# Optimization experiments

Measured on AMD Instinct MI355X. Metric: run time of the kernel, lower is better.

Reference implementation:

```python
import jax, jax.numpy as jnp
import numpy as np

P_X, P_H, P_L, P_VT, P_ET, B = 512, 1024, 4, 512, 256, 512
IN_DIM = P_X + 2 * P_H  # concat([x, prev_time_h, prev_layer_h])


def setup_inputs() -> dict:
    key = jax.random.key(0)
    ks = jax.random.split(key, 10)
    sc_in = 1.0 / np.sqrt(IN_DIM)
    sc_lh = 1.0 / np.sqrt(P_L * P_H)
    return {
        "input_x": jax.random.normal(ks[0], (B, P_X), jnp.float32),
        "h_prev": jax.random.normal(ks[1], (P_L, B, P_H), jnp.float32),
        "c_prev": jax.random.normal(ks[2], (P_L, B, P_H), jnp.float32),
        # stacked gate weights: [L, 4 gates (i,f,o,s), h, in_dim]
        "Wg": jax.random.uniform(ks[3], (P_L, 4, P_H, IN_DIM), jnp.float32, -sc_in, sc_in),
        "bg": jax.random.uniform(ks[4], (P_L, 4, P_H), jnp.float32, -sc_in, sc_in),
        "W_y": jax.random.uniform(ks[5], (P_VT, P_L * P_H), jnp.float32, -sc_lh, sc_lh),
        "b_y": jax.random.uniform(ks[6], (P_VT,), jnp.float32, -sc_lh, sc_lh),
        "W_E": jax.random.uniform(ks[7], (P_ET, P_L * P_H), jnp.float32, -sc_lh, sc_lh),
        "b_E": jax.random.uniform(ks[8], (P_ET,), jnp.float32, -sc_lh, sc_lh),
    }


def _controller(input_x, h_prev, c_prev, Wg, bg):
    prev_layer = jnp.zeros((input_x.shape[0], P_H), input_x.dtype)
    hiddens = []
    for i in range(P_L):  # loop over small fixed layer count
        z = jnp.concatenate([input_x, h_prev[i], prev_layer], axis=-1)  # [B, IN_DIM]
        g = jnp.einsum("bd,ghd->bgh", z, Wg[i]) + bg[i]  # [B, 4, H], one fused GEMM
        i_g = jax.nn.sigmoid(g[:, 0])
        f_g = jax.nn.sigmoid(g[:, 1])
        o_g = jax.nn.sigmoid(g[:, 2])
        s_g = jnp.tanh(g[:, 3])
        c_new = f_g * c_prev[i] + i_g * s_g
        h_new = o_g * jnp.tanh(c_new)
        hiddens.append(h_new)
        prev_layer = h_new
    return jnp.concatenate(hiddens, axis=-1)  # [B, L*H]


def reference(input_x, h_prev, c_prev, Wg, bg, W_y, b_y, W_E, b_E):
    hidden = _controller(input_x, h_prev, c_prev, Wg, bg)
    output = hidden @ W_y.T + b_y      # [B, v_t]
    interface = hidden @ W_E.T + b_E   # [B, E_t]
    return (output, interface)
```

## Files before the change

### kernel.cpp

```cpp
#include <hip/hip_runtime.h>


typedef short    shortx8  __attribute__((ext_vector_type(8)));
typedef float    floatx16 __attribute__((ext_vector_type(16)));

__device__ __forceinline__ unsigned int f2bf1(float x) {
  unsigned int u = __float_as_uint(x);
  return (u + 0x7fffu + ((u >> 16) & 1u)) >> 16;
}
__device__ __forceinline__ unsigned int f2bf2(float lo, float hi) {
  return f2bf1(lo) | (f2bf1(hi) << 16);
}
__device__ __forceinline__ float sigm(float x) { return 1.f / (1.f + __expf(-x)); }
__device__ __forceinline__ float tanh_(float x) { return 1.f - 2.f / (__expf(2.f * x) + 1.f); }

__global__ __launch_bounds__(256) void prep_a0(const float* __restrict__ x,
                                               const float* __restrict__ hp,
                                               unsigned short* __restrict__ A0) {
  const int l   = blockIdx.y;
  const int idx = blockIdx.x * 256 + threadIdx.x;
  const int b   = idx / 192;
  const int kk  = (idx - b * 192) * 8;
  float v[8];
  if (kk < 512) {
    const float* s = x + (size_t)b * 512 + kk;
#pragma unroll
    for (int i = 0; i < 8; ++i) v[i] = s[i];
  } else {
    const float* s = hp + ((size_t)l * 512 + b) * 1024 + (kk - 512);
#pragma unroll
    for (int i = 0; i < 8; ++i) v[i] = s[i];
  }
  uint4 o;
  o.x = f2bf2(v[0], v[1]); o.y = f2bf2(v[2], v[3]);
  o.z = f2bf2(v[4], v[5]); o.w = f2bf2(v[6], v[7]);
  *(uint4*)(A0 + ((size_t)l * 512 + b) * 1536 + kk) = o;
}

__global__ __launch_bounds__(256, 2) void gemm_gates(
    const unsigned short* __restrict__ A0, const float* __restrict__ Wg,
    const float* __restrict__ bg, float* __restrict__ G) {
  __shared__ __align__(16) unsigned short As[2][128 * 64];
  __shared__ __align__(16) unsigned short Bs[2][128 * 64];
  const int tid = threadIdx.x, lane = tid & 63, wave = tid >> 6;
  const int raw   = blockIdx.x + 4 * (blockIdx.y + 32 * blockIdx.z);
  const int xcd   = raw & 7, slot = raw >> 3;
  const int nl    = (slot >> 2) * 8 + xcd;
  const int mbase = (slot & 3) * 128;
  const int nbase = (nl & 31) * 128;
  const int l     = nl >> 5;
  const unsigned short* Ab = A0 + ((size_t)l * 512 + mbase) * 1536;
  const float*          Bb = Wg + (size_t)l * 4096 * 2560 + (size_t)nbase * 2560;
  const int arow = wave * 8 + (lane >> 3);
  const int akg  = lane & 7;

  uint4  apf[4];
  float4 bpf[8];
  auto loadT = [&](int kt) {
    const int kg = kt * 64;
#pragma unroll
    for (int r = 0; r < 4; ++r)
      apf[r] = *(const uint4*)(Ab + (size_t)(arow + r * 32) * 1536 + kg + akg * 8);
#pragma unroll
    for (int j = 0; j < 8; ++j) {
      const int idx = j * 256 + tid;
      bpf[j] = *(const float4*)(Bb + (size_t)(idx >> 4) * 2560 + kg + (idx & 15) * 4);
    }
  };
  auto storeT = [&](int buf) {
#pragma unroll
    for (int r = 0; r < 4; ++r) {
      const int row = arow + r * 32;
      *(uint4*)(&As[buf][row * 64 + ((akg ^ (row & 7)) * 8)]) = apf[r];
    }
#pragma unroll
    for (int j = 0; j < 8; ++j) {
      const int idx = j * 256 + tid;
      const int n = idx >> 4, kc = (idx & 15) * 4;
      uint2 pk;
      pk.x = f2bf2(bpf[j].x, bpf[j].y);
      pk.y = f2bf2(bpf[j].z, bpf[j].w);
      *(uint2*)(&Bs[buf][n * 64 + (((kc >> 3) ^ (n & 7)) * 8) + (kc & 4)]) = pk;
    }
  };

  floatx16 acc[2][2];
#pragma unroll
  for (int a = 0; a < 2; ++a)
#pragma unroll
    for (int b2 = 0; b2 < 2; ++b2)
#pragma unroll
      for (int r = 0; r < 16; ++r) acc[a][b2][r] = 0.f;

  const int wm = (wave >> 1) * 64, wn = (wave & 1) * 64;
  loadT(0);
  storeT(0);
  __syncthreads();
  for (int kt = 0; kt < 24; ++kt) {
    if (kt + 1 < 24) loadT(kt + 1);
    const int cb = kt & 1;
#pragma unroll
    for (int ks = 0; ks < 4; ++ks) {
      const int gb = ks * 2 + (lane >> 5);
      shortx8 af[2], bfv[2];
#pragma unroll
      for (int sm = 0; sm < 2; ++sm) {
        const int row = wm + sm * 32 + (lane & 31);
        af[sm] = *(const shortx8*)(&As[cb][row * 64 + ((gb ^ (row & 7)) * 8)]);
      }
#pragma unroll
      for (int sn = 0; sn < 2; ++sn) {
        const int row = wn + sn * 32 + (lane & 31);
        bfv[sn] = *(const shortx8*)(&Bs[cb][row * 64 + ((gb ^ (row & 7)) * 8)]);
      }
#pragma unroll
      for (int sm = 0; sm < 2; ++sm)
#pragma unroll
        for (int sn = 0; sn < 2; ++sn)
          acc[sm][sn] = __builtin_amdgcn_mfma_f32_32x32x16_bf16(
              af[sm], bfv[sn], acc[sm][sn], 0, 0, 0);
    }
    if (kt + 1 < 24) storeT((kt + 1) & 1);
    __syncthreads();
  }

  const float* bgl = bg + (size_t)l * 4096;
  float* Gl = G + ((size_t)l * 512 + mbase) * 4096;
#pragma unroll
  for (int sm = 0; sm < 2; ++sm)
#pragma unroll
    for (int sn = 0; sn < 2; ++sn) {
      const int col = nbase + wn + sn * 32 + (lane & 31);
      const float bias = bgl[col];
#pragma unroll
      for (int r = 0; r < 16; ++r) {
        const int row = wm + sm * 32 + ((r & 3) + 8 * (r >> 2) + 4 * (lane >> 5));
        Gl[(size_t)row * 4096 + col] = acc[sm][sn][r] + bias;
      }
    }
}

__global__ __launch_bounds__(256) void cell0(const float* __restrict__ G,
                                             const float* __restrict__ cp_l,
                                             unsigned short* __restrict__ hidden) {
  const int idx = (blockIdx.x * 256 + threadIdx.x) * 4;
  const int b = idx >> 10, h = idx & 1023;
  const float* g0 = G + (size_t)b * 4096;
  const float4 vi = *(const float4*)(g0 + h);
  const float4 vf = *(const float4*)(g0 + 1024 + h);
  const float4 vo = *(const float4*)(g0 + 2048 + h);
  const float4 vs = *(const float4*)(g0 + 3072 + h);
  const float4 cp = *(const float4*)(cp_l + (size_t)b * 1024 + h);
  const float gi[4] = {vi.x, vi.y, vi.z, vi.w};
  const float gf[4] = {vf.x, vf.y, vf.z, vf.w};
  const float go[4] = {vo.x, vo.y, vo.z, vo.w};
  const float gs[4] = {vs.x, vs.y, vs.z, vs.w};
  const float cc[4] = {cp.x, cp.y, cp.z, cp.w};
  float hn[4];
#pragma unroll
  for (int j = 0; j < 4; ++j) {
    const float c = sigm(gf[j]) * cc[j] + sigm(gi[j]) * tanh_(gs[j]);
    hn[j] = sigm(go[j]) * tanh_(c);
  }
  uint2 o;
  o.x = f2bf2(hn[0], hn[1]);
  o.y = f2bf2(hn[2], hn[3]);
  *(uint2*)(hidden + (size_t)b * 4096 + h) = o;
}

__global__ __launch_bounds__(512, 2) void gemm_seq_cell(
    const unsigned short* __restrict__ hidden_ro, const float* __restrict__ Wg,
    const float* __restrict__ G, const float* __restrict__ c_prev,
    unsigned short* __restrict__ hidden_w, int l) {
  __shared__ __align__(16) unsigned char raw_lds[49152];
  unsigned short* As = (unsigned short*)raw_lds;
  unsigned short* Bs = (unsigned short*)(raw_lds + 32768);
  float*          Gex = (float*)raw_lds;
  const int tid = threadIdx.x, lane = tid & 63, wave = tid >> 6;
  const int rawb  = blockIdx.x + 4 * blockIdx.y;
  const int xcd   = rawb & 7, slot = rawb >> 3;
  const int mbase = (slot & 3) * 128;
  const int h0    = ((slot >> 2) * 8 + xcd) * 16;
  const unsigned short* Ab = hidden_ro + (size_t)(l - 1) * 1024;
  const float*          Bl = Wg + (size_t)l * 4096 * 2560 + 1536;

  uint4  apf[2];
  float4 bpf[2];
  auto loadT = [&](int kt) {
    const int kg = kt * 64;
#pragma unroll
    for (int r = 0; r < 2; ++r) {
      const int row = (tid >> 3) + r * 64;
      apf[r] = *(const uint4*)(Ab + (size_t)(mbase + row) * 4096 + kg + (tid & 7) * 8);
    }
#pragma unroll
    for (int j = 0; j < 2; ++j) {
      const int idx = j * 512 + tid;
      const int nl = idx >> 4, kc = (idx & 15) * 4;
      const int grow = (nl >> 4) * 1024 + h0 + (nl & 15);
      bpf[j] = *(const float4*)(Bl + (size_t)grow * 2560 + kg + kc);
    }
  };
  auto storeT = [&](int buf) {
#pragma unroll
    for (int r = 0; r < 2; ++r) {
      const int row = (tid >> 3) + r * 64;
      *(uint4*)(&As[buf * 8192 + row * 64 + (((tid & 7) ^ (row & 7)) * 8)]) = apf[r];
    }
#pragma unroll
    for (int j = 0; j < 2; ++j) {
      const int idx = j * 512 + tid;
      const int nl = idx >> 4, kc = (idx & 15) * 4;
      uint2 pk;
      pk.x = f2bf2(bpf[j].x, bpf[j].y);
      pk.y = f2bf2(bpf[j].z, bpf[j].w);
      *(uint2*)(&Bs[buf * 4096 + nl * 64 + (((kc >> 3) ^ (nl & 7)) * 8) + (kc & 4)]) = pk;
    }
  };

  floatx16 acc;
#pragma unroll
  for (int r = 0; r < 16; ++r) acc[r] = 0.f;
  const int wm = (wave & 3) * 32, wn = (wave >> 2) * 32;

  loadT(0);
  storeT(0);
  __syncthreads();
  for (int kt = 0; kt < 16; ++kt) {
    if (kt + 1 < 16) loadT(kt + 1);
    const int cb = kt & 1;
    const int rowa = wm + (lane & 31);
    const int rowb = wn + (lane & 31);
#pragma unroll
    for (int ks = 0; ks < 4; ++ks) {
      const int gb = ks * 2 + (lane >> 5);
      const shortx8 af = *(const shortx8*)(&As[cb * 8192 + rowa * 64 + ((gb ^ (rowa & 7)) * 8)]);
      const shortx8 bfv = *(const shortx8*)(&Bs[cb * 4096 + rowb * 64 + ((gb ^ (rowb & 7)) * 8)]);
      acc = __builtin_amdgcn_mfma_f32_32x32x16_bf16(af, bfv, acc, 0, 0, 0);
    }
    if (kt + 1 < 16) storeT((kt + 1) & 1);
    __syncthreads();
  }

  {
    const int col = wn + (lane & 31);
#pragma unroll
    for (int r = 0; r < 16; ++r) {
      const int row = wm + ((r & 3) + 8 * (r >> 2) + 4 * (lane >> 5));
      Gex[row * 65 + col] = acc[r];
    }
  }
  __syncthreads();

  const int hh = tid & 15, q = tid >> 4;
#pragma unroll
  for (int bi = 0; bi < 4; ++bi) {
    const int bl = bi * 32 + q;
    const int b  = mbase + bl;
    const int hg = h0 + hh;
    const float* Gb = G + ((size_t)l * 512 + b) * 4096;
    float gv[4];
#pragma unroll
    for (int g = 0; g < 4; ++g)
      gv[g] = Gex[bl * 65 + g * 16 + hh] + Gb[g * 1024 + hg];
    const float c_old = c_prev[((size_t)l * 512 + b) * 1024 + hg];
    const float c  = sigm(gv[1]) * c_old + sigm(gv[0]) * tanh_(gv[3]);
    const float hn = sigm(gv[2]) * tanh_(c);
    hidden_w[(size_t)b * 4096 + l * 1024 + hg] = (unsigned short)f2bf1(hn);
  }
}

__global__ __launch_bounds__(256) void gemm_heads(
    const unsigned short* __restrict__ A, const float* __restrict__ Wy,
    const float* __restrict__ WE, float* __restrict__ Cp) {
  __shared__ __align__(16) unsigned short As[2][128 * 64];
  __shared__ __align__(16) unsigned short Bs[2][128 * 64];
  const int tid = threadIdx.x, lane = tid & 63, wave = tid >> 6;
  const int rawb = blockIdx.x + 8 * (blockIdx.y + 6 * blockIdx.z);
  const int xcd  = rawb & 7, slot = rawb >> 3;
  const int pair = (slot >> 2) * 8 + xcd;
  const int mbase  = (slot & 3) * 128;
  const int ksplit = pair & 7;
  const int nt     = pair >> 3;
  const int nbase  = nt * 128;
  const float* Bb = (nt < 4) ? (Wy + (size_t)nbase * 4096)
                             : (WE + (size_t)(nbase - 512) * 4096);
  const int k0 = ksplit * 512;
  const unsigned short* Ab = A + (size_t)mbase * 4096;
  const int arow = wave * 8 + (lane >> 3);
  const int akg  = lane & 7;

  uint4  apf[4];
  float4 bpf[8];
  auto loadT = [&](int kt) {
    const int kg = k0 + kt * 64;
#pragma unroll
    for (int r = 0; r < 4; ++r)
      apf[r] = *(const uint4*)(Ab + (size_t)(arow + r * 32) * 4096 + kg + akg * 8);
#pragma unroll
    for (int j = 0; j < 8; ++j) {
      const int idx = j * 256 + tid;
      bpf[j] = *(const float4*)(Bb + (size_t)(idx >> 4) * 4096 + kg + (idx & 15) * 4);
    }
  };
  auto storeT = [&](int buf) {
#pragma unroll
    for (int r = 0; r < 4; ++r) {
      const int row = arow + r * 32;
      *(uint4*)(&As[buf][row * 64 + ((akg ^ (row & 7)) * 8)]) = apf[r];
    }
#pragma unroll
    for (int j = 0; j < 8; ++j) {
      const int idx = j * 256 + tid;
      const int n = idx >> 4, kc = (idx & 15) * 4;
      uint2 pk;
      pk.x = f2bf2(bpf[j].x, bpf[j].y);
      pk.y = f2bf2(bpf[j].z, bpf[j].w);
      *(uint2*)(&Bs[buf][n * 64 + (((kc >> 3) ^ (n & 7)) * 8) + (kc & 4)]) = pk;
    }
  };

  floatx16 acc[2][2];
#pragma unroll
  for (int a = 0; a < 2; ++a)
#pragma unroll
    for (int b2 = 0; b2 < 2; ++b2)
#pragma unroll
      for (int r = 0; r < 16; ++r) acc[a][b2][r] = 0.f;
  const int wm = (wave >> 1) * 64, wn = (wave & 1) * 64;

  loadT(0);
  storeT(0);
  __syncthreads();
  for (int kt = 0; kt < 8; ++kt) {
    if (kt + 1 < 8) loadT(kt + 1);
    const int cb = kt & 1;
#pragma unroll
    for (int ks = 0; ks < 4; ++ks) {
      const int gb = ks * 2 + (lane >> 5);
      shortx8 af[2], bfv[2];
#pragma unroll
      for (int sm = 0; sm < 2; ++sm) {
        const int row = wm + sm * 32 + (lane & 31);
        af[sm] = *(const shortx8*)(&As[cb][row * 64 + ((gb ^ (row & 7)) * 8)]);
      }
#pragma unroll
      for (int sn = 0; sn < 2; ++sn) {
        const int row = wn + sn * 32 + (lane & 31);
        bfv[sn] = *(const shortx8*)(&Bs[cb][row * 64 + ((gb ^ (row & 7)) * 8)]);
      }
#pragma unroll
      for (int sm = 0; sm < 2; ++sm)
#pragma unroll
        for (int sn = 0; sn < 2; ++sn)
          acc[sm][sn] = __builtin_amdgcn_mfma_f32_32x32x16_bf16(
              af[sm], bfv[sn], acc[sm][sn], 0, 0, 0);
    }
    if (kt + 1 < 8) storeT((kt + 1) & 1);
    __syncthreads();
  }

  float* Co = Cp + (size_t)ksplit * 512 * 768;
#pragma unroll
  for (int sm = 0; sm < 2; ++sm)
#pragma unroll
    for (int sn = 0; sn < 2; ++sn) {
      const int col = nbase + wn + sn * 32 + (lane & 31);
#pragma unroll
      for (int r = 0; r < 16; ++r) {
        const int row = mbase + wm + sm * 32 +
                        ((r & 3) + 8 * (r >> 2) + 4 * (lane >> 5));
        Co[(size_t)row * 768 + col] = acc[sm][sn][r];
      }
    }
}

__global__ __launch_bounds__(256) void head_reduce(
    const float* __restrict__ hp, const float* __restrict__ b_y,
    const float* __restrict__ b_E, float* __restrict__ out) {
  const int n = blockIdx.x * 256 + threadIdx.x;
  const int b = blockIdx.y;
  float s = 0.f;
#pragma unroll
  for (int ks = 0; ks < 8; ++ks)
    s += hp[(size_t)ks * 512 * 768 + (size_t)b * 768 + n];
  if (n < 512)
    out[(size_t)b * 512 + n] = s + b_y[n];
  else
    out[(size_t)512 * 512 + (size_t)b * 256 + (n - 512)] = s + b_E[n - 512];
}

extern "C" void kernel_launch(void* const* d_in, const int* in_sizes, int n_in,
                              void* d_out, int out_size, void* d_ws, size_t ws_size,
                              hipStream_t stream) {
  const float* x      = (const float*)d_in[0];
  const float* h_prev = (const float*)d_in[1];
  const float* c_prev = (const float*)d_in[2];
  const float* Wg     = (const float*)d_in[3];
  const float* bg     = (const float*)d_in[4];
  const float* W_y    = (const float*)d_in[5];
  const float* b_y    = (const float*)d_in[6];
  const float* W_E    = (const float*)d_in[7];
  const float* b_E    = (const float*)d_in[8];

  char* ws = (char*)d_ws;
  unsigned short* A0     = (unsigned short*)(ws + 0);
  float*          G      = (float*)(ws + 6291456);
  unsigned short* hidden = (unsigned short*)(ws + 39845888);
  float*          hpart  = (float*)(ws + 44040192);

  prep_a0<<<dim3(384, 4), 256, 0, stream>>>(x, h_prev, A0);
  gemm_gates<<<dim3(4, 32, 4), 256, 0, stream>>>(A0, Wg, bg, G);
  cell0<<<512, 256, 0, stream>>>(G, c_prev, hidden);
  for (int l = 1; l < 4; ++l)
    gemm_seq_cell<<<dim3(4, 64), 512, 0, stream>>>(hidden, Wg, G, c_prev,
                                                   hidden, l);
  gemm_heads<<<dim3(8, 6, 4), 256, 0, stream>>>(hidden, W_y, W_E, hpart);
  head_reduce<<<dim3(3, 512), 256, 0, stream>>>(hpart, b_y, b_E, (float*)d_out);
}
```

Before: 420.4 us.

## Prefetch two K-tiles ahead in GEMMs and enlarge gate GEMM tile to 256x128

All three GEMM kernels now keep two register prefetch sets and load tiles two steps ahead, with a manually double-unrolled main loop, to hide more global-load latency behind the MFMA work. The gate GEMM is also restructured to 512 threads with a 256x128 output tile and a 1-D grid of 256 blocks. The grid maps one layer and M half to each XCD so each XCD reuses the same A rows. This costs more registers and LDS per block, which may lower occupancy, and the gate grid shrinks from 512 to 256 blocks.

```diff
diff --git a/kernel.cpp b/kernel.cpp
--- a/kernel.cpp
+++ b/kernel.cpp
@@ -37,50 +37,50 @@
   *(uint4*)(A0 + ((size_t)l * 512 + b) * 1536 + kk) = o;
 }
 
-__global__ __launch_bounds__(256, 2) void gemm_gates(
+__global__ __launch_bounds__(512, 2) void gemm_gates(
     const unsigned short* __restrict__ A0, const float* __restrict__ Wg,
     const float* __restrict__ bg, float* __restrict__ G) {
-  __shared__ __align__(16) unsigned short As[2][128 * 64];
+  __shared__ __align__(16) unsigned short As[2][256 * 64];
   __shared__ __align__(16) unsigned short Bs[2][128 * 64];
   const int tid = threadIdx.x, lane = tid & 63, wave = tid >> 6;
-  const int raw   = blockIdx.x + 4 * (blockIdx.y + 32 * blockIdx.z);
-  const int xcd   = raw & 7, slot = raw >> 3;
-  const int nl    = (slot >> 2) * 8 + xcd;
-  const int mbase = (slot & 3) * 128;
-  const int nbase = (nl & 31) * 128;
-  const int l     = nl >> 5;
+  const int bid   = blockIdx.x;
+  const int xcd   = bid & 7;
+  const int n     = bid >> 3;
+  const int l     = xcd >> 1;
+  const int mbase = (xcd & 1) * 256;
+  const int nbase = n * 128;
   const unsigned short* Ab = A0 + ((size_t)l * 512 + mbase) * 1536;
   const float*          Bb = Wg + (size_t)l * 4096 * 2560 + (size_t)nbase * 2560;
-  const int arow = wave * 8 + (lane >> 3);
-  const int akg  = lane & 7;
-
-  uint4  apf[4];
-  float4 bpf[8];
-  auto loadT = [&](int kt) {
+  const int arow = tid >> 3;
+  const int akg  = tid & 7;
+
+  uint4  apfA[4], apfB[4];
+  float4 bpfA[4], bpfB[4];
+  auto loadT = [&](uint4 (&ap)[4], float4 (&bp)[4], int kt) {
     const int kg = kt * 64;
 #pragma unroll
     for (int r = 0; r < 4; ++r)
-      apf[r] = *(const uint4*)(Ab + (size_t)(arow + r * 32) * 1536 + kg + akg * 8);
-#pragma unroll
-    for (int j = 0; j < 8; ++j) {
-      const int idx = j * 256 + tid;
-      bpf[j] = *(const float4*)(Bb + (size_t)(idx >> 4) * 2560 + kg + (idx & 15) * 4);
-    }
-  };
-  auto storeT = [&](int buf) {
+      ap[r] = *(const uint4*)(Ab + (size_t)(arow + r * 64) * 1536 + kg + akg * 8);
+#pragma unroll
+    for (int j = 0; j < 4; ++j) {
+      const int idx = j * 512 + tid;
+      bp[j] = *(const float4*)(Bb + (size_t)(idx >> 4) * 2560 + kg + (idx & 15) * 4);
+    }
+  };
+  auto storeT = [&](uint4 (&ap)[4], float4 (&bp)[4], int buf) {
 #pragma unroll
     for (int r = 0; r < 4; ++r) {
-      const int row = arow + r * 32;
-      *(uint4*)(&As[buf][row * 64 + ((akg ^ (row & 7)) * 8)]) = apf[r];
-    }
-#pragma unroll
-    for (int j = 0; j < 8; ++j) {
-      const int idx = j * 256 + tid;
-      const int n = idx >> 4, kc = (idx & 15) * 4;
+      const int row = arow + r * 64;
+      *(uint4*)(&As[buf][row * 64 + ((akg ^ (row & 7)) * 8)]) = ap[r];
+    }
+#pragma unroll
+    for (int j = 0; j < 4; ++j) {
+      const int idx = j * 512 + tid;
+      const int nr = idx >> 4, kc = (idx & 15) * 4;
       uint2 pk;
-      pk.x = f2bf2(bpf[j].x, bpf[j].y);
-      pk.y = f2bf2(bpf[j].z, bpf[j].w);
-      *(uint2*)(&Bs[buf][n * 64 + (((kc >> 3) ^ (n & 7)) * 8) + (kc & 4)]) = pk;
+      pk.x = f2bf2(bp[j].x, bp[j].y);
+      pk.y = f2bf2(bp[j].z, bp[j].w);
+      *(uint2*)(&Bs[buf][nr * 64 + (((kc >> 3) ^ (nr & 7)) * 8) + (kc & 4)]) = pk;
     }
   };
 
@@ -92,13 +92,8 @@
 #pragma unroll
       for (int r = 0; r < 16; ++r) acc[a][b2][r] = 0.f;
 
-  const int wm = (wave >> 1) * 64, wn = (wave & 1) * 64;
-  loadT(0);
-  storeT(0);
-  __syncthreads();
-  for (int kt = 0; kt < 24; ++kt) {
-    if (kt + 1 < 24) loadT(kt + 1);
-    const int cb = kt & 1;
+  const int wm = (wave & 3) * 64, wn = (wave >> 2) * 64;
+  auto compute = [&](int cb) {
 #pragma unroll
     for (int ks = 0; ks < 4; ++ks) {
       const int gb = ks * 2 + (lane >> 5);
@@ -120,7 +115,22 @@
           acc[sm][sn] = __builtin_amdgcn_mfma_f32_32x32x16_bf16(
               af[sm], bfv[sn], acc[sm][sn], 0, 0, 0);
     }
-    if (kt + 1 < 24) storeT((kt + 1) & 1);
+  };
+
+  loadT(apfA, bpfA, 0);
+  loadT(apfB, bpfB, 1);
+  storeT(apfA, bpfA, 0);
+  __syncthreads();
+#pragma unroll 1
+  for (int kt2 = 0; kt2 < 12; ++kt2) {
+    const int kt = kt2 * 2;
+    if (kt + 2 < 24) loadT(apfA, bpfA, kt + 2);
+    compute(0);
+    storeT(apfB, bpfB, 1);
+    __syncthreads();
+    if (kt + 3 < 24) loadT(apfB, bpfB, kt + 3);
+    compute(1);
+    if (kt + 2 < 24) storeT(apfA, bpfA, 0);
     __syncthreads();
   }
 
@@ -184,36 +194,36 @@
   const unsigned short* Ab = hidden_ro + (size_t)(l - 1) * 1024;
   const float*          Bl = Wg + (size_t)l * 4096 * 2560 + 1536;
 
-  uint4  apf[2];
-  float4 bpf[2];
-  auto loadT = [&](int kt) {
+  uint4  apfA[2], apfB[2];
+  float4 bpfA[2], bpfB[2];
+  auto loadT = [&](uint4 (&ap)[2], float4 (&bp)[2], int kt) {
     const int kg = kt * 64;
 #pragma unroll
     for (int r = 0; r < 2; ++r) {
       const int row = (tid >> 3) + r * 64;
-      apf[r] = *(const uint4*)(Ab + (size_t)(mbase + row) * 4096 + kg + (tid & 7) * 8);
+      ap[r] = *(const uint4*)(Ab + (size_t)(mbase + row) * 4096 + kg + (tid & 7) * 8);
     }
 #pragma unroll
     for (int j = 0; j < 2; ++j) {
       const int idx = j * 512 + tid;
       const int nl = idx >> 4, kc = (idx & 15) * 4;
       const int grow = (nl >> 4) * 1024 + h0 + (nl & 15);
-      bpf[j] = *(const float4*)(Bl + (size_t)grow * 2560 + kg + kc);
-    }
-  };
-  auto storeT = [&](int buf) {
+      bp[j] = *(const float4*)(Bl + (size_t)grow * 2560 + kg + kc);
+    }
+  };
+  auto storeT = [&](uint4 (&ap)[2], float4 (&bp)[2], int buf) {
 #pragma unroll
     for (int r = 0; r < 2; ++r) {
       const int row = (tid >> 3) + r * 64;
-      *(uint4*)(&As[buf * 8192 + row * 64 + (((tid & 7) ^ (row & 7)) * 8)]) = apf[r];
+      *(uint4*)(&As[buf * 8192 + row * 64 + (((tid & 7) ^ (row & 7)) * 8)]) = ap[r];
     }
 #pragma unroll
     for (int j = 0; j < 2; ++j) {
       const int idx = j * 512 + tid;
       const int nl = idx >> 4, kc = (idx & 15) * 4;
       uint2 pk;
-      pk.x = f2bf2(bpf[j].x, bpf[j].y);
-      pk.y = f2bf2(bpf[j].z, bpf[j].w);
+      pk.x = f2bf2(bp[j].x, bp[j].y);
+      pk.y = f2bf2(bp[j].z, bp[j].w);
       *(uint2*)(&Bs[buf * 4096 + nl * 64 + (((kc >> 3) ^ (nl & 7)) * 8) + (kc & 4)]) = pk;
     }
   };
@@ -222,15 +232,10 @@
 #pragma unroll
   for (int r = 0; r < 16; ++r) acc[r] = 0.f;
   const int wm = (wave & 3) * 32, wn = (wave >> 2) * 32;
-
-  loadT(0);
-  storeT(0);
-  __syncthreads();
-  for (int kt = 0; kt < 16; ++kt) {
-    if (kt + 1 < 16) loadT(kt + 1);
-    const int cb = kt & 1;
-    const int rowa = wm + (lane & 31);
-    const int rowb = wn + (lane & 31);
+  const int rowa = wm + (lane & 31);
+  const int rowb = wn + (lane & 31);
+
+  auto compute = [&](int cb) {
 #pragma unroll
     for (int ks = 0; ks < 4; ++ks) {
       const int gb = ks * 2 + (lane >> 5);
@@ -238,7 +243,22 @@
       const shortx8 bfv = *(const shortx8*)(&Bs[cb * 4096 + rowb * 64 + ((gb ^ (rowb & 7)) * 8)]);
       acc = __builtin_amdgcn_mfma_f32_32x32x16_bf16(af, bfv, acc, 0, 0, 0);
     }
-    if (kt + 1 < 16) storeT((kt + 1) & 1);
+  };
+
+  loadT(apfA, bpfA, 0);
+  loadT(apfB, bpfB, 1);
+  storeT(apfA, bpfA, 0);
+  __syncthreads();
+#pragma unroll 1
+  for (int kt2 = 0; kt2 < 8; ++kt2) {
+    const int kt = kt2 * 2;
+    if (kt + 2 < 16) loadT(apfA, bpfA, kt + 2);
+    compute(0);
+    storeT(apfB, bpfB, 1);
+    __syncthreads();
+    if (kt + 3 < 16) loadT(apfB, bpfB, kt + 3);
+    compute(1);
+    if (kt + 2 < 16) storeT(apfA, bpfA, 0);
     __syncthreads();
   }
 
@@ -270,7 +290,7 @@
   }
 }
 
-__global__ __launch_bounds__(256) void gemm_heads(
+__global__ __launch_bounds__(256, 2) void gemm_heads(
     const unsigned short* __restrict__ A, const float* __restrict__ Wy,
     const float* __restrict__ WE, float* __restrict__ Cp) {
   __shared__ __align__(16) unsigned short As[2][128 * 64];
@@ -290,32 +310,32 @@
   const int arow = wave * 8 + (lane >> 3);
   const int akg  = lane & 7;
 
-  uint4  apf[4];
-  float4 bpf[8];
-  auto loadT = [&](int kt) {
+  uint4  apfA[4], apfB[4];
+  float4 bpfA[8], bpfB[8];
+  auto loadT = [&](uint4 (&ap)[4], float4 (&bp)[8], int kt) {
     const int kg = k0 + kt * 64;
 #pragma unroll
     for (int r = 0; r < 4; ++r)
-      apf[r] = *(const uint4*)(Ab + (size_t)(arow + r * 32) * 4096 + kg + akg * 8);
+      ap[r] = *(const uint4*)(Ab + (size_t)(arow + r * 32) * 4096 + kg + akg * 8);
 #pragma unroll
     for (int j = 0; j < 8; ++j) {
       const int idx = j * 256 + tid;
-      bpf[j] = *(const float4*)(Bb + (size_t)(idx >> 4) * 4096 + kg + (idx & 15) * 4);
-    }
-  };
-  auto storeT = [&](int buf) {
+      bp[j] = *(const float4*)(Bb + (size_t)(idx >> 4) * 4096 + kg + (idx & 15) * 4);
+    }
+  };
+  auto storeT = [&](uint4 (&ap)[4], float4 (&bp)[8], int buf) {
 #pragma unroll
     for (int r = 0; r < 4; ++r) {
       const int row = arow + r * 32;
-      *(uint4*)(&As[buf][row * 64 + ((akg ^ (row & 7)) * 8)]) = apf[r];
+      *(uint4*)(&As[buf][row * 64 + ((akg ^ (row & 7)) * 8)]) = ap[r];
     }
 #pragma unroll
     for (int j = 0; j < 8; ++j) {
       const int idx = j * 256 + tid;
       const int n = idx >> 4, kc = (idx & 15) * 4;
       uint2 pk;
-      pk.x = f2bf2(bpf[j].x, bpf[j].y);
-      pk.y = f2bf2(bpf[j].z, bpf[j].w);
+      pk.x = f2bf2(bp[j].x, bp[j].y);
+      pk.y = f2bf2(bp[j].z, bp[j].w);
       *(uint2*)(&Bs[buf][n * 64 + (((kc >> 3) ^ (n & 7)) * 8) + (kc & 4)]) = pk;
     }
   };
@@ -329,12 +349,7 @@
       for (int r = 0; r < 16; ++r) acc[a][b2][r] = 0.f;
   const int wm = (wave >> 1) * 64, wn = (wave & 1) * 64;
 
-  loadT(0);
-  storeT(0);
-  __syncthreads();
-  for (int kt = 0; kt < 8; ++kt) {
-    if (kt + 1 < 8) loadT(kt + 1);
-    const int cb = kt & 1;
+  auto compute = [&](int cb) {
 #pragma unroll
     for (int ks = 0; ks < 4; ++ks) {
       const int gb = ks * 2 + (lane >> 5);
@@ -356,7 +371,22 @@
           acc[sm][sn] = __builtin_amdgcn_mfma_f32_32x32x16_bf16(
               af[sm], bfv[sn], acc[sm][sn], 0, 0, 0);
     }
-    if (kt + 1 < 8) storeT((kt + 1) & 1);
+  };
+
+  loadT(apfA, bpfA, 0);
+  loadT(apfB, bpfB, 1);
+  storeT(apfA, bpfA, 0);
+  __syncthreads();
+#pragma unroll 1
+  for (int kt2 = 0; kt2 < 4; ++kt2) {
+    const int kt = kt2 * 2;
+    if (kt + 2 < 8) loadT(apfA, bpfA, kt + 2);
+    compute(0);
+    storeT(apfB, bpfB, 1);
+    __syncthreads();
+    if (kt + 3 < 8) loadT(apfB, bpfB, kt + 3);
+    compute(1);
+    if (kt + 2 < 8) storeT(apfA, bpfA, 0);
     __syncthreads();
   }
 
@@ -410,7 +440,7 @@
   float*          hpart  = (float*)(ws + 44040192);
 
   prep_a0<<<dim3(384, 4), 256, 0, stream>>>(x, h_prev, A0);
-  gemm_gates<<<dim3(4, 32, 4), 256, 0, stream>>>(A0, Wg, bg, G);
+  gemm_gates<<<dim3(256), 512, 0, stream>>>(A0, Wg, bg, G);
   cell0<<<512, 256, 0, stream>>>(G, c_prev, hidden);
   for (int l = 1; l < 4; ++l)
     gemm_seq_cell<<<dim3(4, 64), 512, 0, stream>>>(hidden, Wg, G, c_prev,
```

After: 444.9 us. +5.8%, slower.

## Pre-convert sequential-layer weights to bf16 and stream them in LDS-free kernel

Applied to the files above, without the earlier changes.

Adds a kernel that converts the previous-layer slice of the gate weights for layers 1-3 into a compact bf16 buffer each call. The per-layer sequential GEMM+cell kernel is replaced by an LDS-free version: each wave computes a 16x16 tile per gate with 16x16x32 bf16 MFMA, prefetching operands from global memory into registers four k-steps ahead. This removes the fp32 weight loads with in-loop conversion, the LDS staging and the block barriers, and uses more blocks. In exchange it adds an extra conversion pass over the weights and puts the bf16 buffer in the same workspace region as hpart, which is safe only because the head GEMM runs after it on the same stream.

```diff
diff --git a/kernel.cpp b/kernel.cpp
--- a/kernel.cpp
+++ b/kernel.cpp
@@ -2,6 +2,7 @@
 
 
 typedef short    shortx8  __attribute__((ext_vector_type(8)));
+typedef float    floatx4  __attribute__((ext_vector_type(4)));
 typedef float    floatx16 __attribute__((ext_vector_type(16)));
 
 __device__ __forceinline__ unsigned int f2bf1(float x) {
@@ -35,6 +36,22 @@
   o.x = f2bf2(v[0], v[1]); o.y = f2bf2(v[2], v[3]);
   o.z = f2bf2(v[4], v[5]); o.w = f2bf2(v[6], v[7]);
   *(uint4*)(A0 + ((size_t)l * 512 + b) * 1536 + kk) = o;
+}
+
+__global__ __launch_bounds__(256) void conv_wseq(const float* __restrict__ Wg,
+                                                 unsigned short* __restrict__ Wseq) {
+  const int idx = blockIdx.x * 256 + threadIdx.x;
+  const int row = idx >> 7;
+  const int k0  = (idx & 127) * 8;
+  const int l   = (row >> 12) + 1;
+  const int n   = row & 4095;
+  const float* s = Wg + (size_t)l * 4096 * 2560 + (size_t)n * 2560 + 1536 + k0;
+  const float4 v0 = *(const float4*)(s);
+  const float4 v1 = *(const float4*)(s + 4);
+  uint4 o;
+  o.x = f2bf2(v0.x, v0.y); o.y = f2bf2(v0.z, v0.w);
+  o.z = f2bf2(v1.x, v1.y); o.w = f2bf2(v1.z, v1.w);
+  *(uint4*)(Wseq + (size_t)row * 1024 + k0) = o;
 }
 
 __global__ __launch_bounds__(256, 2) void gemm_gates(
@@ -168,105 +185,93 @@
   *(uint2*)(hidden + (size_t)b * 4096 + h) = o;
 }
 
-__global__ __launch_bounds__(512, 2) void gemm_seq_cell(
-    const unsigned short* __restrict__ hidden_ro, const float* __restrict__ Wg,
+__global__ __launch_bounds__(256) void seq_stream(
+    const unsigned short* __restrict__ hidden_ro,
+    const unsigned short* __restrict__ Wseq,
     const float* __restrict__ G, const float* __restrict__ c_prev,
     unsigned short* __restrict__ hidden_w, int l) {
-  __shared__ __align__(16) unsigned char raw_lds[49152];
-  unsigned short* As = (unsigned short*)raw_lds;
-  unsigned short* Bs = (unsigned short*)(raw_lds + 32768);
-  float*          Gex = (float*)raw_lds;
-  const int tid = threadIdx.x, lane = tid & 63, wave = tid >> 6;
-  const int rawb  = blockIdx.x + 4 * blockIdx.y;
-  const int xcd   = rawb & 7, slot = rawb >> 3;
-  const int mbase = (slot & 3) * 128;
-  const int h0    = ((slot >> 2) * 8 + xcd) * 16;
-  const unsigned short* Ab = hidden_ro + (size_t)(l - 1) * 1024;
-  const float*          Bl = Wg + (size_t)l * 4096 * 2560 + 1536;
-
-  uint4  apf[2];
-  float4 bpf[2];
-  auto loadT = [&](int kt) {
-    const int kg = kt * 64;
-#pragma unroll
-    for (int r = 0; r < 2; ++r) {
-      const int row = (tid >> 3) + r * 64;
-      apf[r] = *(const uint4*)(Ab + (size_t)(mbase + row) * 4096 + kg + (tid & 7) * 8);
-    }
-#pragma unroll
-    for (int j = 0; j < 2; ++j) {
-      const int idx = j * 512 + tid;
-      const int nl = idx >> 4, kc = (idx & 15) * 4;
-      const int grow = (nl >> 4) * 1024 + h0 + (nl & 15);
-      bpf[j] = *(const float4*)(Bl + (size_t)grow * 2560 + kg + kc);
-    }
-  };
-  auto storeT = [&](int buf) {
-#pragma unroll
-    for (int r = 0; r < 2; ++r) {
-      const int row = (tid >> 3) + r * 64;
-      *(uint4*)(&As[buf * 8192 + row * 64 + (((tid & 7) ^ (row & 7)) * 8)]) = apf[r];
-    }
-#pragma unroll
-    for (int j = 0; j < 2; ++j) {
-      const int idx = j * 512 + tid;
-      const int nl = idx >> 4, kc = (idx & 15) * 4;
-      uint2 pk;
-      pk.x = f2bf2(bpf[j].x, bpf[j].y);
-      pk.y = f2bf2(bpf[j].z, bpf[j].w);
-      *(uint2*)(&Bs[buf * 4096 + nl * 64 + (((kc >> 3) ^ (nl & 7)) * 8) + (kc & 4)]) = pk;
-    }
-  };
-
-  floatx16 acc;
-#pragma unroll
-  for (int r = 0; r < 16; ++r) acc[r] = 0.f;
-  const int wm = (wave & 3) * 32, wn = (wave >> 2) * 32;
-
-  loadT(0);
-  storeT(0);
-  __syncthreads();
-  for (int kt = 0; kt < 16; ++kt) {
-    if (kt + 1 < 16) loadT(kt + 1);
-    const int cb = kt & 1;
-    const int rowa = wm + (lane & 31);
-    const int rowb = wn + (lane & 31);
-#pragma unroll
-    for (int ks = 0; ks < 4; ++ks) {
-      const int gb = ks * 2 + (lane >> 5);
-      const shortx8 af = *(const shortx8*)(&As[cb * 8192 + rowa * 64 + ((gb ^ (rowa & 7)) * 8)]);
-      const shortx8 bfv = *(const shortx8*)(&Bs[cb * 4096 + rowb * 64 + ((gb ^ (rowb & 7)) * 8)]);
-      acc = __builtin_amdgcn_mfma_f32_32x32x16_bf16(af, bfv, acc, 0, 0, 0);
-    }
-    if (kt + 1 < 16) storeT((kt + 1) & 1);
-    __syncthreads();
-  }
-
-  {
-    const int col = wn + (lane & 31);
-#pragma unroll
-    for (int r = 0; r < 16; ++r) {
-      const int row = wm + ((r & 3) + 8 * (r >> 2) + 4 * (lane >> 5));
-      Gex[row * 65 + col] = acc[r];
-    }
-  }
-  __syncthreads();
-
-  const int hh = tid & 15, q = tid >> 4;
-#pragma unroll
-  for (int bi = 0; bi < 4; ++bi) {
-    const int bl = bi * 32 + q;
-    const int b  = mbase + bl;
-    const int hg = h0 + hh;
-    const float* Gb = G + ((size_t)l * 512 + b) * 4096;
-    float gv[4];
-#pragma unroll
-    for (int g = 0; g < 4; ++g)
-      gv[g] = Gex[bl * 65 + g * 16 + hh] + Gb[g * 1024 + hg];
-    const float c_old = c_prev[((size_t)l * 512 + b) * 1024 + hg];
-    const float c  = sigm(gv[1]) * c_old + sigm(gv[0]) * tanh_(gv[3]);
-    const float hn = sigm(gv[2]) * tanh_(c);
-    hidden_w[(size_t)b * 4096 + l * 1024 + hg] = (unsigned short)f2bf1(hn);
+  const int tid = threadIdx.x, lane = tid & 63, wv = tid >> 6;
+  const int bid = blockIdx.x;
+  const int x   = bid & 7;
+  const int mg  = (bid >> 3) & 7;
+  const int t   = bid >> 6;
+  const int ht  = x * 8 + t;
+  const int mt  = mg * 4 + wv;
+  const int mb  = mt * 16, h0 = ht * 16;
+  const int lrow = lane & 15, lg = lane >> 4;
+
+  const unsigned short* Ab = hidden_ro + (size_t)(mb + lrow) * 4096
+                             + (size_t)(l - 1) * 1024 + lg * 8;
+  const unsigned short* Bb = Wseq + (size_t)(l - 1) * 4194304
+                             + (size_t)(h0 + lrow) * 1024 + lg * 8;
+
+  const int brow = mb + lg * 4;
+  const int hg   = h0 + lrow;
+  float gvv[4][4];
+  float cold[4];
+#pragma unroll
+  for (int r = 0; r < 4; ++r) {
+    const float* Gb = G + ((size_t)l * 512 + brow + r) * 4096 + hg;
+#pragma unroll
+    for (int g = 0; g < 4; ++g) gvv[g][r] = Gb[g * 1024];
+    cold[r] = c_prev[((size_t)l * 512 + brow + r) * 1024 + hg];
+  }
+
+  floatx4 acc0, acc1, acc2, acc3;
+#pragma unroll
+  for (int r = 0; r < 4; ++r) { acc0[r] = 0.f; acc1[r] = 0.f; acc2[r] = 0.f; acc3[r] = 0.f; }
+
+  shortx8 a0, a1, a2, a3;
+  shortx8 b00, b01, b02, b03;
+  shortx8 b10, b11, b12, b13;
+  shortx8 b20, b21, b22, b23;
+  shortx8 b30, b31, b32, b33;
+
+#define LD_SET(ai, b0_, b1_, b2_, b3_, kt)                                   \
+  {                                                                          \
+    const int ko = (kt) * 32;                                                \
+    ai  = *(const shortx8*)(Ab + ko);                                        \
+    b0_ = *(const shortx8*)(Bb + ko);                                        \
+    b1_ = *(const shortx8*)(Bb + 1048576 + ko);                              \
+    b2_ = *(const shortx8*)(Bb + 2097152 + ko);                              \
+    b3_ = *(const shortx8*)(Bb + 3145728 + ko);                              \
+  }
+#define C_SET(ai, b0_, b1_, b2_, b3_)                                        \
+  {                                                                          \
+    acc0 = __builtin_amdgcn_mfma_f32_16x16x32_bf16(ai, b0_, acc0, 0, 0, 0);  \
+    acc1 = __builtin_amdgcn_mfma_f32_16x16x32_bf16(ai, b1_, acc1, 0, 0, 0);  \
+    acc2 = __builtin_amdgcn_mfma_f32_16x16x32_bf16(ai, b2_, acc2, 0, 0, 0);  \
+    acc3 = __builtin_amdgcn_mfma_f32_16x16x32_bf16(ai, b3_, acc3, 0, 0, 0);  \
+  }
+
+  LD_SET(a0, b00, b01, b02, b03, 0)
+  LD_SET(a1, b10, b11, b12, b13, 1)
+  LD_SET(a2, b20, b21, b22, b23, 2)
+  LD_SET(a3, b30, b31, b32, b33, 3)
+#pragma unroll 1
+  for (int kt4 = 0; kt4 < 8; ++kt4) {
+    const int kt = kt4 * 4;
+    C_SET(a0, b00, b01, b02, b03)
+    if (kt + 4 < 32) LD_SET(a0, b00, b01, b02, b03, kt + 4)
+    C_SET(a1, b10, b11, b12, b13)
+    if (kt + 5 < 32) LD_SET(a1, b10, b11, b12, b13, kt + 5)
+    C_SET(a2, b20, b21, b22, b23)
+    if (kt + 6 < 32) LD_SET(a2, b20, b21, b22, b23, kt + 6)
+    C_SET(a3, b30, b31, b32, b33)
+    if (kt + 7 < 32) LD_SET(a3, b30, b31, b32, b33, kt + 7)
+  }
+#undef LD_SET
+#undef C_SET
+
+#pragma unroll
+  for (int r = 0; r < 4; ++r) {
+    const float gi = acc0[r] + gvv[0][r];
+    const float gf = acc1[r] + gvv[1][r];
+    const float go = acc2[r] + gvv[2][r];
+    const float gs = acc3[r] + gvv[3][r];
+    const float c  = sigm(gf) * cold[r] + sigm(gi) * tanh_(gs);
+    const float hn = sigm(go) * tanh_(c);
+    hidden_w[(size_t)(brow + r) * 4096 + l * 1024 + hg] = (unsigned short)f2bf1(hn);
   }
 }
 
@@ -407,14 +412,16 @@
   unsigned short* A0     = (unsigned short*)(ws + 0);
   float*          G      = (float*)(ws + 6291456);
   unsigned short* hidden = (unsigned short*)(ws + 39845888);
+  unsigned short* Wseq   = (unsigned short*)(ws + 44040192);
   float*          hpart  = (float*)(ws + 44040192);
 
+  conv_wseq<<<dim3(6144), 256, 0, stream>>>(Wg, Wseq);
   prep_a0<<<dim3(384, 4), 256, 0, stream>>>(x, h_prev, A0);
   gemm_gates<<<dim3(4, 32, 4), 256, 0, stream>>>(A0, Wg, bg, G);
   cell0<<<512, 256, 0, stream>>>(G, c_prev, hidden);
   for (int l = 1; l < 4; ++l)
-    gemm_seq_cell<<<dim3(4, 64), 512, 0, stream>>>(hidden, Wg, G, c_prev,
-                                                   hidden, l);
+    seq_stream<<<dim3(512), 256, 0, stream>>>(hidden, Wseq, G, c_prev,
+                                              hidden, l);
   gemm_heads<<<dim3(8, 6, 4), 256, 0, stream>>>(hidden, W_y, W_E, hpart);
   head_reduce<<<dim3(3, 512), 256, 0, stream>>>(hpart, b_y, b_E, (float*)d_out);
 }
```

New measurement: 460.3 us. 9.5% more time.
